# Optimization experiments

Hardware: AMD Instinct MI355X
Metric: run time of the kernel (lower is better)

The kernel has to match this reference:

```python
import jax, jax.numpy as jnp
import numpy as np

E = 1024      # embed_dim
H = 16        # num_heads
HD = E // H   # head_dim = 64


def setup_inputs() -> dict:
    key = jax.random.key(0)
    ks = jax.random.split(key, 8)
    T, B, S = 1024, 4, 1024
    return {
        "query": jax.random.normal(ks[0], (T, B, E), jnp.float32),
        "key": jax.random.normal(ks[1], (S, B, E), jnp.float32),
        "value": jax.random.normal(ks[2], (S, B, E), jnp.float32),
        "attn_mask": jax.random.normal(ks[3], (T, S), jnp.float32),
        "key_padding_mask": jax.random.randint(ks[4], (B, S), 0, 2, jnp.int32),
        "in_proj_weight": jax.random.normal(ks[5], (3 * E, E), jnp.float32) * 0.02,
        "in_proj_bias": jnp.zeros((3 * E,), jnp.float32),
        "out_w": jax.random.normal(ks[6], (E, E), jnp.float32) * 0.02,
        "out_b": jnp.zeros((E,), jnp.float32),
    }


def reference(query, key, value, attn_mask, key_padding_mask,
              in_proj_weight, in_proj_bias, out_w, out_b):
    T, B, _ = query.shape
    S = key.shape[0]
    w_q, w_k, w_v = jnp.split(in_proj_weight, 3, axis=0)   # each [E, E]
    b_q, b_k, b_v = jnp.split(in_proj_bias, 3, axis=0)
    q = query @ w_q.T + b_q                                # [T, B, E]
    k = key @ w_k.T + b_k                                  # [S, B, E]
    v = value @ w_v.T + b_v                                # [S, B, E]
    # [len, B, E] -> [B*H, len, HD]
    q = q.reshape(T, B * H, HD).transpose(1, 0, 2) / jnp.sqrt(jnp.float32(HD))
    k = k.reshape(S, B * H, HD).transpose(1, 0, 2)
    v = v.reshape(S, B * H, HD).transpose(1, 0, 2)
    scores = jnp.einsum('bth,bsh->bts', q, k)              # [B*H, T, S]
    scores = scores + attn_mask[None]                      # float additive mask
    pad = key_padding_mask.astype(bool)                    # [B, S]
    pad = jnp.broadcast_to(pad[:, None, None, :], (B, H, 1, S)).reshape(B * H, 1, S)
    scores = jnp.where(pad, -jnp.inf, scores)
    weights = jax.nn.softmax(scores, axis=-1)              # dropout p=0 -> identity
    out = jnp.einsum('bts,bsh->bth', weights, v)           # [B*H, T, HD]
    out = out.transpose(1, 0, 2).reshape(T, B, E)
    out = out @ out_w.T + out_b
    weights_avg = weights.reshape(B, H, T, S).mean(axis=1) # sum/H == mean
    return out, weights_avg
```

## Files before the change

kernel.cpp:

```cpp
#include <hip/hip_runtime.h>
#include <stdint.h>

typedef short bf16x8 __attribute__((ext_vector_type(8)));
typedef float f32x4  __attribute__((ext_vector_type(4)));

#define LOG2E_F 1.4426950408889634f
#define QSCALE_F 0.1803368801111204f

__device__ __forceinline__ unsigned short f2bf(float f) {
    unsigned int u = __float_as_uint(f);
    return (unsigned short)((u + 0x7FFFu + ((u >> 16) & 1u)) >> 16);
}

__device__ __forceinline__ unsigned short f2bfu(float f) {
    return (unsigned short)((__float_as_uint(f) + 0x8000u) >> 16);
}

__device__ __forceinline__ uint4 pack8(float4 a, float4 b) {
    union { unsigned short us[8]; uint4 v; } p;
    p.us[0] = f2bf(a.x); p.us[1] = f2bf(a.y); p.us[2] = f2bf(a.z); p.us[3] = f2bf(a.w);
    p.us[4] = f2bf(b.x); p.us[5] = f2bf(b.y); p.us[6] = f2bf(b.z); p.us[7] = f2bf(b.w);
    return p.v;
}

__global__ __launch_bounds__(256)
void cvt_kernel(const float* __restrict__ q, const float* __restrict__ k,
                const float* __restrict__ v, const float* __restrict__ w,
                const float* __restrict__ ow,
                uint4* __restrict__ Xb, uint4* __restrict__ Wb, uint4* __restrict__ OWb)
{
    const unsigned g = blockIdx.x * 256 + threadIdx.x;
    const float* src;
    uint4* dst;
    if (g < 1572864u) {
        dst = Xb + g;
        if (g < 524288u)        src = q + (size_t)g * 8;
        else if (g < 1048576u)  src = k + (size_t)(g - 524288u) * 8;
        else                    src = v + (size_t)(g - 1048576u) * 8;
    } else if (g < 1966080u) {
        src = w + (size_t)(g - 1572864u) * 8;
        dst = Wb + (g - 1572864u);
    } else {
        src = ow + (size_t)(g - 1966080u) * 8;
        dst = OWb + (g - 1966080u);
    }
    float4 a = *(const float4*)src;
    float4 b = *(const float4*)(src + 4);
    *dst = pack8(a, b);
}

__global__ __launch_bounds__(256)
void mtr_kernel(const float* __restrict__ m, float* __restrict__ mt)
{
    __shared__ float tile[64][65];
    const int bt = (blockIdx.x & 15) << 6;
    const int bs = (blockIdx.x >> 4) << 6;
    const int tx = threadIdx.x & 63;
    const int ty = threadIdx.x >> 6;
#pragma unroll
    for (int i = 0; i < 64; i += 4)
        tile[ty + i][tx] = m[(size_t)(bt + ty + i) * 1024 + bs + tx];
    __syncthreads();
#pragma unroll
    for (int i = 0; i < 64; i += 4)
        mt[(size_t)(bs + ty + i) * 1024 + bt + tx] = tile[tx][ty + i];
}

__global__ __launch_bounds__(256)
void qkv_proj_kernel(const unsigned short* __restrict__ Xb, const unsigned short* __restrict__ Wb,
                     const float* __restrict__ bias,
                     unsigned short* __restrict__ Qb, unsigned short* __restrict__ Kb,
                     unsigned short* __restrict__ Vtb)
{
    const int z = blockIdx.z;
    const int j   = blockIdx.x;
    const int xcd = j & 7, idx = j >> 3;
    const int row0 = ((xcd << 2) + (idx >> 3)) * 128;
    const int col0 = (idx & 7) * 128;
    const int wofs = z << 10;

    const unsigned short* A = Xb + (size_t)z * 4194304;
    const unsigned short* B = Wb;

    __shared__ __align__(16) unsigned short As[128 * 72];
    __shared__ __align__(16) unsigned short Bs[128 * 72];

    const int tid  = threadIdx.x;
    const int lane = tid & 63;
    const int wv   = tid >> 6;
    const int wr   = wv >> 1, wc = wv & 1;

    const f32x4 zero4 = {0.f, 0.f, 0.f, 0.f};
    f32x4 acc[4][4];
#pragma unroll
    for (int m = 0; m < 4; ++m)
#pragma unroll
        for (int n = 0; n < 4; ++n) acc[m][n] = zero4;

    const int srow = tid >> 1;
    const int scol = (tid & 1) << 5;
    const int arow = wr * 64 + (lane & 15);
    const int brow = wc * 64 + (lane & 15);
    const int kof  = (lane >> 4) << 3;

    const unsigned short* pa = A + (size_t)(row0 + srow) * 1024 + scol;
    const unsigned short* pb = B + (size_t)(wofs + col0 + srow) * 1024 + scol;
    uint4 ra0 = *(const uint4*)(pa + 0),  ra1 = *(const uint4*)(pa + 8);
    uint4 ra2 = *(const uint4*)(pa + 16), ra3 = *(const uint4*)(pa + 24);
    uint4 rb0 = *(const uint4*)(pb + 0),  rb1 = *(const uint4*)(pb + 8);
    uint4 rb2 = *(const uint4*)(pb + 16), rb3 = *(const uint4*)(pb + 24);

    for (int k0 = 0; k0 < 1024; k0 += 64) {
        __syncthreads();
        *(uint4*)&As[srow * 72 + scol]      = ra0;
        *(uint4*)&As[srow * 72 + scol + 8]  = ra1;
        *(uint4*)&As[srow * 72 + scol + 16] = ra2;
        *(uint4*)&As[srow * 72 + scol + 24] = ra3;
        *(uint4*)&Bs[srow * 72 + scol]      = rb0;
        *(uint4*)&Bs[srow * 72 + scol + 8]  = rb1;
        *(uint4*)&Bs[srow * 72 + scol + 16] = rb2;
        *(uint4*)&Bs[srow * 72 + scol + 24] = rb3;
        __syncthreads();

        if (k0 < 960) {
            pa = A + (size_t)(row0 + srow) * 1024 + k0 + 64 + scol;
            pb = B + (size_t)(wofs + col0 + srow) * 1024 + k0 + 64 + scol;
            ra0 = *(const uint4*)(pa + 0);  ra1 = *(const uint4*)(pa + 8);
            ra2 = *(const uint4*)(pa + 16); ra3 = *(const uint4*)(pa + 24);
            rb0 = *(const uint4*)(pb + 0);  rb1 = *(const uint4*)(pb + 8);
            rb2 = *(const uint4*)(pb + 16); rb3 = *(const uint4*)(pb + 24);
        }

#pragma unroll
        for (int kk = 0; kk < 2; ++kk) {
            bf16x8 af[4], bfr[4];
#pragma unroll
            for (int m = 0; m < 4; ++m)
                af[m] = *(const bf16x8*)&As[(arow + m * 16) * 72 + kk * 32 + kof];
#pragma unroll
            for (int n = 0; n < 4; ++n)
                bfr[n] = *(const bf16x8*)&Bs[(brow + n * 16) * 72 + kk * 32 + kof];
#pragma unroll
            for (int m = 0; m < 4; ++m)
#pragma unroll
                for (int n = 0; n < 4; ++n)
                    acc[m][n] = __builtin_amdgcn_mfma_f32_16x16x32_bf16(af[m], bfr[n], acc[m][n], 0, 0, 0);
        }
    }

    const int ccol = lane & 15;
    const int crow = (lane >> 4) << 2;
#pragma unroll
    for (int n = 0; n < 4; ++n) {
        const int gc   = col0 + wc * 64 + n * 16 + ccol;
        const float bv = bias[wofs + gc];
        const int head = gc >> 6, d = gc & 63;
#pragma unroll
        for (int m = 0; m < 4; ++m) {
#pragma unroll
            for (int r = 0; r < 4; ++r) {
                const int gr = row0 + wr * 64 + m * 16 + crow + r;
                const int t  = gr >> 2, b = gr & 3;
                const int bh = (b << 4) + head;
                float vv = acc[m][n][r] + bv;
                if (z == 0)      Qb [((size_t)bh << 16) + ((size_t)t << 6) + d]  = f2bf(vv * QSCALE_F);
                else if (z == 1) Kb [((size_t)bh << 16) + ((size_t)t << 6) + d]  = f2bf(vv);
                else             Vtb[((size_t)bh << 16) + ((size_t)d << 10) + t] = f2bf(vv);
            }
        }
    }
}

__global__ __launch_bounds__(512)
void flash_kernel(const unsigned short* __restrict__ Qb, const unsigned short* __restrict__ Kb,
                  const unsigned short* __restrict__ Vtb, const float* __restrict__ maskT,
                  const int* __restrict__ padmask,
                  float* __restrict__ rl_buf, unsigned short* __restrict__ attn_out)
{
    const int j   = blockIdx.x;
    const int xcd = j & 7, idx = j >> 3;
    const int bh  = xcd * 8 + (idx >> 3);
    const int t0  = (idx & 7) << 7;
    const int b   = bh >> 4, h = bh & 15;

    __shared__ __align__(16) unsigned short Ks[2][2][64 * 72];
    __shared__ __align__(16) unsigned short Vs[2][2][64 * 72];

    const int tid  = threadIdx.x;
    const int lane = tid & 63;
    const int wv   = tid >> 6;
    const int kof  = (lane >> 4) << 3;
    const int c16  = lane & 15;
    const int g4   = (lane >> 4) << 2;

    const unsigned short* Qbase = Qb  + ((size_t)bh << 16);
    const unsigned short* Kbase = Kb  + ((size_t)bh << 16);
    const unsigned short* Vbase = Vtb + ((size_t)bh << 16);

    bf16x8 qf[2];
#pragma unroll
    for (int kk = 0; kk < 2; ++kk)
        qf[kk] = *(const bf16x8*)(Qbase + ((size_t)(t0 + wv * 16 + c16) << 6) + kk * 32 + kof);

    const bf16x8 ones = {16256, 16256, 16256, 16256, 16256, 16256, 16256, 16256};

    const f32x4 zero4 = {0.f, 0.f, 0.f, 0.f};
    f32x4 acco[4];
#pragma unroll
    for (int nd = 0; nd < 4; ++nd) acco[nd] = zero4;
    f32x4 acc_l = zero4;

    const int srow_st = tid >> 3;
    const int scol_st = (tid & 7) << 3;

    const int bb  = scol_st & 31;
    const int hh  = scol_st & 32;
    const int cL  = hh + ((bb & 15) >> 2) * 8 + (bb >> 4) * 4;
    const int bb4 = bb + 4;
    const int cH  = hh + ((bb4 & 15) >> 2) * 8 + (bb4 >> 4) * 4;

    const int tr2 = t0 + wv * 16 + c16;

    const unsigned short* kp = Kbase + ((size_t)srow_st << 6) + scol_st;
    const unsigned short* vp = Vbase + ((size_t)srow_st << 10) + scol_st;
    uint4 kA = *(const uint4*)kp;
    uint4 kB = *(const uint4*)(kp + 4096);
    uint4 vA = *(const uint4*)vp;
    uint4 vB = *(const uint4*)(vp + 64);

    {
        *(uint4*)&Ks[0][0][srow_st * 72 + scol_st] = kA;
        *(uint4*)&Ks[0][1][srow_st * 72 + scol_st] = kB;
        uint2 lo, hi;
        lo.x = vA.x; lo.y = vA.y; hi.x = vA.z; hi.y = vA.w;
        *(uint2*)&Vs[0][0][srow_st * 72 + cL] = lo;
        *(uint2*)&Vs[0][0][srow_st * 72 + cH] = hi;
        lo.x = vB.x; lo.y = vB.y; hi.x = vB.z; hi.y = vB.w;
        *(uint2*)&Vs[0][1][srow_st * 72 + cL] = lo;
        *(uint2*)&Vs[0][1][srow_st * 72 + cH] = hi;
    }
    kp = Kbase + ((size_t)(128 + srow_st) << 6) + scol_st;
    vp = Vbase + ((size_t)srow_st << 10) + 128 + scol_st;
    kA = *(const uint4*)kp;
    kB = *(const uint4*)(kp + 4096);
    vA = *(const uint4*)vp;
    vB = *(const uint4*)(vp + 64);
    __syncthreads();

    for (int rd = 0; rd < 8; ++rd) {
        const int cur = rd & 1;
        const int s0  = rd << 7;

        if (rd < 7) {
            *(uint4*)&Ks[cur ^ 1][0][srow_st * 72 + scol_st] = kA;
            *(uint4*)&Ks[cur ^ 1][1][srow_st * 72 + scol_st] = kB;
            uint2 lo, hi;
            lo.x = vA.x; lo.y = vA.y; hi.x = vA.z; hi.y = vA.w;
            *(uint2*)&Vs[cur ^ 1][0][srow_st * 72 + cL] = lo;
            *(uint2*)&Vs[cur ^ 1][0][srow_st * 72 + cH] = hi;
            lo.x = vB.x; lo.y = vB.y; hi.x = vB.z; hi.y = vB.w;
            *(uint2*)&Vs[cur ^ 1][1][srow_st * 72 + cL] = lo;
            *(uint2*)&Vs[cur ^ 1][1][srow_st * 72 + cH] = hi;
        }
        if (rd < 6) {
            const int sn = s0 + 256;
            kp = Kbase + ((size_t)(sn + srow_st) << 6) + scol_st;
            vp = Vbase + ((size_t)srow_st << 10) + sn + scol_st;
            kA = *(const uint4*)kp;
            kB = *(const uint4*)(kp + 4096);
            vA = *(const uint4*)vp;
            vB = *(const uint4*)(vp + 64);
        }

        f32x4 accsA[4], accsB[4];
#pragma unroll
        for (int n = 0; n < 4; ++n) { accsA[n] = zero4; accsB[n] = zero4; }
        __builtin_amdgcn_s_setprio(1);
#pragma unroll
        for (int n = 0; n < 4; ++n) {
            bf16x8 kfA0 = *(const bf16x8*)&Ks[cur][0][(n * 16 + c16) * 72 + kof];
            bf16x8 kfA1 = *(const bf16x8*)&Ks[cur][0][(n * 16 + c16) * 72 + 32 + kof];
            accsA[n] = __builtin_amdgcn_mfma_f32_16x16x32_bf16(kfA0, qf[0], accsA[n], 0, 0, 0);
            accsA[n] = __builtin_amdgcn_mfma_f32_16x16x32_bf16(kfA1, qf[1], accsA[n], 0, 0, 0);
            bf16x8 kfB0 = *(const bf16x8*)&Ks[cur][1][(n * 16 + c16) * 72 + kof];
            bf16x8 kfB1 = *(const bf16x8*)&Ks[cur][1][(n * 16 + c16) * 72 + 32 + kof];
            accsB[n] = __builtin_amdgcn_mfma_f32_16x16x32_bf16(kfB0, qf[0], accsB[n], 0, 0, 0);
            accsB[n] = __builtin_amdgcn_mfma_f32_16x16x32_bf16(kfB1, qf[1], accsB[n], 0, 0, 0);
        }
        __builtin_amdgcn_s_setprio(0);

#pragma unroll
        for (int tile = 0; tile < 2; ++tile) {
            const int s0t = s0 + tile * 64;
            f32x4* accs = tile ? accsB : accsA;

            float mk[4][4];
            int4 pd[4];
#pragma unroll
            for (int n = 0; n < 4; ++n) {
                const int srow = s0t + n * 16 + g4;
                pd[n] = *(const int4*)(padmask + (b << 10) + srow);
#pragma unroll
                for (int r = 0; r < 4; ++r)
                    mk[n][r] = maskT[(size_t)(srow + r) * 1024 + tr2];
            }

            union { unsigned short us[16]; bf16x8 v[2]; } pk;
#pragma unroll
            for (int n = 0; n < 4; ++n) {
                float x0 = fmaf(mk[n][0], LOG2E_F, accs[n][0]);
                float x1 = fmaf(mk[n][1], LOG2E_F, accs[n][1]);
                float x2 = fmaf(mk[n][2], LOG2E_F, accs[n][2]);
                float x3 = fmaf(mk[n][3], LOG2E_F, accs[n][3]);
                if (pd[n].x) x0 = -1e30f;
                if (pd[n].y) x1 = -1e30f;
                if (pd[n].z) x2 = -1e30f;
                if (pd[n].w) x3 = -1e30f;
                pk.us[n * 4 + 0] = f2bfu(__builtin_amdgcn_exp2f(x0));
                pk.us[n * 4 + 1] = f2bfu(__builtin_amdgcn_exp2f(x1));
                pk.us[n * 4 + 2] = f2bfu(__builtin_amdgcn_exp2f(x2));
                pk.us[n * 4 + 3] = f2bfu(__builtin_amdgcn_exp2f(x3));
            }

            __builtin_amdgcn_s_setprio(1);
#pragma unroll
            for (int hhh = 0; hhh < 2; ++hhh) {
                bf16x8 pf = pk.v[hhh];
#pragma unroll
                for (int nd = 0; nd < 4; ++nd) {
                    bf16x8 vf = *(const bf16x8*)&Vs[cur][tile][(nd * 16 + c16) * 72 + hhh * 32 + kof];
                    acco[nd] = __builtin_amdgcn_mfma_f32_16x16x32_bf16(pf, vf, acco[nd], 0, 0, 0);
                }
                acc_l = __builtin_amdgcn_mfma_f32_16x16x32_bf16(pf, ones, acc_l, 0, 0, 0);
            }
            __builtin_amdgcn_s_setprio(0);
        }

        if (rd < 7) __syncthreads();
    }

#pragma unroll
    for (int r = 0; r < 4; ++r) {
        const int t = t0 + wv * 16 + g4 + r;
        const float rl = 1.0f / acc_l[r];
        if (c16 == 0)
            rl_buf[(bh << 10) + t] = rl;
#pragma unroll
        for (int nd = 0; nd < 4; ++nd) {
            const int d = nd * 16 + c16;
            attn_out[((size_t)t * 4 + b) * 1024 + h * 64 + d] = f2bf(acco[nd][r] * rl);
        }
    }
}

__global__ __launch_bounds__(256)
void wavg_kernel(const unsigned short* __restrict__ Qb, const unsigned short* __restrict__ Kb,
                 const float* __restrict__ attn_mask, const int* __restrict__ padmask,
                 const float* __restrict__ rl_buf, float* __restrict__ wout)
{
    const int j   = blockIdx.x;
    const int xcd = j & 7;
    const int b   = xcd >> 1;
    const int rr  = ((j >> 3) << 1) + (xcd & 1);
    const int t0  = (rr >> 4) << 6;
    const int s0  = (rr & 15) << 6;

    __shared__ __align__(16) unsigned short Qs[64 * 72];
    __shared__ __align__(16) unsigned short Ks2[64 * 72];

    const int tid  = threadIdx.x;
    const int lane = tid & 63;
    const int wv   = tid >> 6;
    const int wr   = wv >> 1, wc = wv & 1;
    const int kof  = (lane >> 4) << 3;
    const int srow_st = tid >> 2;
    const int scol_st = (tid & 3) << 4;

    const int t_base = t0 + wr * 32 + ((lane >> 4) << 2);
    const int s_base = s0 + wc * 32 + (lane & 15);

    int pad2[2];
#pragma unroll
    for (int nn = 0; nn < 2; ++nn) pad2[nn] = padmask[(b << 10) + s_base + nn * 16];

    float maskv[2][2][4];
#pragma unroll
    for (int mm = 0; mm < 2; ++mm)
#pragma unroll
        for (int r = 0; r < 4; ++r)
#pragma unroll
            for (int nn = 0; nn < 2; ++nn)
                maskv[mm][nn][r] = attn_mask[(size_t)(t_base + mm * 16 + r) * 1024 + s_base + nn * 16] * LOG2E_F;

    float wsum[2][2][4];
#pragma unroll
    for (int mm = 0; mm < 2; ++mm)
#pragma unroll
        for (int nn = 0; nn < 2; ++nn)
#pragma unroll
            for (int r = 0; r < 4; ++r) wsum[mm][nn][r] = 0.f;

    for (int h = 0; h < 16; ++h) {
        const int bh = (b << 4) + h;
        __syncthreads();
        {
            const unsigned short* qp = Qb + ((size_t)bh << 16) + ((size_t)(t0 + srow_st) << 6) + scol_st;
            *(uint4*)&Qs[srow_st * 72 + scol_st]     = *(const uint4*)qp;
            *(uint4*)&Qs[srow_st * 72 + scol_st + 8] = *(const uint4*)(qp + 8);
            const unsigned short* kp = Kb + ((size_t)bh << 16) + ((size_t)(s0 + srow_st) << 6) + scol_st;
            *(uint4*)&Ks2[srow_st * 72 + scol_st]     = *(const uint4*)kp;
            *(uint4*)&Ks2[srow_st * 72 + scol_st + 8] = *(const uint4*)(kp + 8);
        }
        __syncthreads();

        float rlv[2][4];
#pragma unroll
        for (int mm = 0; mm < 2; ++mm)
#pragma unroll
            for (int r = 0; r < 4; ++r)
                rlv[mm][r] = rl_buf[(bh << 10) + t_base + mm * 16 + r];

        const f32x4 zero4 = {0.f, 0.f, 0.f, 0.f};
        f32x4 accs[2][2];
#pragma unroll
        for (int mm = 0; mm < 2; ++mm)
#pragma unroll
            for (int nn = 0; nn < 2; ++nn) accs[mm][nn] = zero4;
#pragma unroll
        for (int nn = 0; nn < 2; ++nn) {
            bf16x8 kf0 = *(const bf16x8*)&Ks2[(wc * 32 + nn * 16 + (lane & 15)) * 72 + kof];
            bf16x8 kf1 = *(const bf16x8*)&Ks2[(wc * 32 + nn * 16 + (lane & 15)) * 72 + 32 + kof];
#pragma unroll
            for (int mm = 0; mm < 2; ++mm) {
                bf16x8 qf0 = *(const bf16x8*)&Qs[(wr * 32 + mm * 16 + (lane & 15)) * 72 + kof];
                bf16x8 qf1 = *(const bf16x8*)&Qs[(wr * 32 + mm * 16 + (lane & 15)) * 72 + 32 + kof];
                accs[mm][nn] = __builtin_amdgcn_mfma_f32_16x16x32_bf16(qf0, kf0, accs[mm][nn], 0, 0, 0);
                accs[mm][nn] = __builtin_amdgcn_mfma_f32_16x16x32_bf16(qf1, kf1, accs[mm][nn], 0, 0, 0);
            }
        }
#pragma unroll
        for (int mm = 0; mm < 2; ++mm)
#pragma unroll
            for (int nn = 0; nn < 2; ++nn)
#pragma unroll
                for (int r = 0; r < 4; ++r)
                    if (!pad2[nn]) {
                        float x = accs[mm][nn][r] + maskv[mm][nn][r];
                        wsum[mm][nn][r] += __builtin_amdgcn_exp2f(x) * rlv[mm][r];
                    }
    }

#pragma unroll
    for (int mm = 0; mm < 2; ++mm)
#pragma unroll
        for (int nn = 0; nn < 2; ++nn)
#pragma unroll
            for (int r = 0; r < 4; ++r)
                wout[((size_t)b << 20) + (size_t)(t_base + mm * 16 + r) * 1024 + s_base + nn * 16]
                    = wsum[mm][nn][r] * 0.0625f;
}

__global__ __launch_bounds__(256)
void out_proj_kernel(const unsigned short* __restrict__ A, const unsigned short* __restrict__ Wb,
                     const float* __restrict__ bias, float* __restrict__ out)
{
    const int j   = blockIdx.x;
    const int xcd = j & 7, idx = j >> 3;
    const int row0 = ((xcd << 2) + (idx >> 3)) * 128;
    const int col0 = (idx & 7) * 128;

    __shared__ __align__(16) unsigned short As[128 * 72];
    __shared__ __align__(16) unsigned short Bs[128 * 72];

    const int tid  = threadIdx.x;
    const int lane = tid & 63;
    const int wv   = tid >> 6;
    const int wr   = wv >> 1, wc = wv & 1;

    const f32x4 zero4 = {0.f, 0.f, 0.f, 0.f};
    f32x4 acc[4][4];
#pragma unroll
    for (int m = 0; m < 4; ++m)
#pragma unroll
        for (int n = 0; n < 4; ++n) acc[m][n] = zero4;

    const int srow = tid >> 1;
    const int scol = (tid & 1) << 5;
    const int arow = wr * 64 + (lane & 15);
    const int brow = wc * 64 + (lane & 15);
    const int kof  = (lane >> 4) << 3;

    const unsigned short* pa = A  + (size_t)(row0 + srow) * 1024 + scol;
    const unsigned short* pb = Wb + (size_t)(col0 + srow) * 1024 + scol;
    uint4 ra0 = *(const uint4*)(pa + 0),  ra1 = *(const uint4*)(pa + 8);
    uint4 ra2 = *(const uint4*)(pa + 16), ra3 = *(const uint4*)(pa + 24);
    uint4 rb0 = *(const uint4*)(pb + 0),  rb1 = *(const uint4*)(pb + 8);
    uint4 rb2 = *(const uint4*)(pb + 16), rb3 = *(const uint4*)(pb + 24);

    for (int k0 = 0; k0 < 1024; k0 += 64) {
        __syncthreads();
        *(uint4*)&As[srow * 72 + scol]      = ra0;
        *(uint4*)&As[srow * 72 + scol + 8]  = ra1;
        *(uint4*)&As[srow * 72 + scol + 16] = ra2;
        *(uint4*)&As[srow * 72 + scol + 24] = ra3;
        *(uint4*)&Bs[srow * 72 + scol]      = rb0;
        *(uint4*)&Bs[srow * 72 + scol + 8]  = rb1;
        *(uint4*)&Bs[srow * 72 + scol + 16] = rb2;
        *(uint4*)&Bs[srow * 72 + scol + 24] = rb3;
        __syncthreads();

        if (k0 < 960) {
            pa = A  + (size_t)(row0 + srow) * 1024 + k0 + 64 + scol;
            pb = Wb + (size_t)(col0 + srow) * 1024 + k0 + 64 + scol;
            ra0 = *(const uint4*)(pa + 0);  ra1 = *(const uint4*)(pa + 8);
            ra2 = *(const uint4*)(pa + 16); ra3 = *(const uint4*)(pa + 24);
            rb0 = *(const uint4*)(pb + 0);  rb1 = *(const uint4*)(pb + 8);
            rb2 = *(const uint4*)(pb + 16); rb3 = *(const uint4*)(pb + 24);
        }

#pragma unroll
        for (int kk = 0; kk < 2; ++kk) {
            bf16x8 af[4], bfr[4];
#pragma unroll
            for (int m = 0; m < 4; ++m)
                af[m] = *(const bf16x8*)&As[(arow + m * 16) * 72 + kk * 32 + kof];
#pragma unroll
            for (int n = 0; n < 4; ++n)
                bfr[n] = *(const bf16x8*)&Bs[(brow + n * 16) * 72 + kk * 32 + kof];
#pragma unroll
            for (int m = 0; m < 4; ++m)
#pragma unroll
                for (int n = 0; n < 4; ++n)
                    acc[m][n] = __builtin_amdgcn_mfma_f32_16x16x32_bf16(af[m], bfr[n], acc[m][n], 0, 0, 0);
        }
    }

    const int ccol = lane & 15;
    const int crow = (lane >> 4) << 2;
#pragma unroll
    for (int n = 0; n < 4; ++n) {
        const int gc   = col0 + wc * 64 + n * 16 + ccol;
        const float bv = bias[gc];
#pragma unroll
        for (int m = 0; m < 4; ++m) {
#pragma unroll
            for (int r = 0; r < 4; ++r) {
                const int gr = row0 + wr * 64 + m * 16 + crow + r;
                out[(size_t)gr * 1024 + gc] = acc[m][n][r] + bv;
            }
        }
    }
}

extern "C" void kernel_launch(void* const* d_in, const int* in_sizes, int n_in,
                              void* d_out, int out_size, void* d_ws, size_t ws_size,
                              hipStream_t stream)
{
    const float* query     = (const float*)d_in[0];
    const float* key       = (const float*)d_in[1];
    const float* value     = (const float*)d_in[2];
    const float* attn_mask = (const float*)d_in[3];
    const int*   padmask   = (const int*)  d_in[4];
    const float* in_proj_w = (const float*)d_in[5];
    const float* in_proj_b = (const float*)d_in[6];
    const float* out_w     = (const float*)d_in[7];
    const float* out_b     = (const float*)d_in[8];

    float* out  = (float*)d_out;
    float* wavg = out + 4194304;

    char* ws = (char*)d_ws;
    unsigned short* Qb     = (unsigned short*)(ws);
    unsigned short* Kb     = (unsigned short*)(ws + 8388608);
    unsigned short* Vtb    = (unsigned short*)(ws + 16777216);
    unsigned short* Xb     = (unsigned short*)(ws + 25165824);
    unsigned short* attn_o = (unsigned short*)(ws + 25165824);
    float*          maskT  = (float*)(ws + 33554432);
    unsigned short* Wb     = (unsigned short*)(ws + 50331648);
    unsigned short* OWb    = (unsigned short*)(ws + 56623104);
    float*          rl_buf = (float*)(ws + 58720256);

    cvt_kernel<<<dim3(8192), 256, 0, stream>>>(query, key, value, in_proj_w, out_w,
                                               (uint4*)Xb, (uint4*)Wb, (uint4*)OWb);
    qkv_proj_kernel<<<dim3(256, 1, 3), 256, 0, stream>>>(Xb, Wb, in_proj_b, Qb, Kb, Vtb);
    mtr_kernel<<<dim3(256), 256, 0, stream>>>(attn_mask, maskT);
    flash_kernel<<<dim3(512), 512, 0, stream>>>(Qb, Kb, Vtb, maskT, padmask,
                                                rl_buf, attn_o);
    wavg_kernel<<<dim3(1024), 256, 0, stream>>>(Qb, Kb, attn_mask, padmask,
                                                rl_buf, wavg);
    out_proj_kernel<<<dim3(256), 256, 0, stream>>>(attn_o, OWb, out_b, out);
}
```

Before: 156.2 us.

## Interleave transposed mask layout for vector loads and double-buffer wavg Q/K tiles

The mask transpose kernel now writes an interleaved layout that groups four consecutive s rows per t, so the attention kernel fetches its four mask values with one float4 load instead of four strided scalar loads. The wavg kernel double-buffers the Q/K shared tiles, keeping the next head's data in registers and cutting the barriers per head from two to one, so global loads overlap with MFMA and exp work. The cost is twice the shared memory in wavg and extra live registers, which may lower occupancy.

```diff
diff --git a/kernel.cpp b/kernel.cpp
--- a/kernel.cpp
+++ b/kernel.cpp
@@ -62,8 +62,10 @@
         tile[ty + i][tx] = m[(size_t)(bt + ty + i) * 1024 + bs + tx];
     __syncthreads();
 #pragma unroll
-    for (int i = 0; i < 64; i += 4)
-        mt[(size_t)(bs + ty + i) * 1024 + bt + tx] = tile[tx][ty + i];
+    for (int i = 0; i < 64; i += 4) {
+        const int s = bs + ty + i;
+        mt[(size_t)(s >> 2) * 4096 + (bt + tx) * 4 + (s & 3)] = tile[tx][ty + i];
+    }
 }
 
 __global__ __launch_bounds__(256)
@@ -294,24 +296,22 @@
             const int s0t = s0 + tile * 64;
             f32x4* accs = tile ? accsB : accsA;
 
-            float mk[4][4];
+            float4 mk[4];
             int4 pd[4];
 #pragma unroll
             for (int n = 0; n < 4; ++n) {
                 const int srow = s0t + n * 16 + g4;
                 pd[n] = *(const int4*)(padmask + (b << 10) + srow);
-#pragma unroll
-                for (int r = 0; r < 4; ++r)
-                    mk[n][r] = maskT[(size_t)(srow + r) * 1024 + tr2];
+                mk[n] = *(const float4*)(maskT + (size_t)(srow >> 2) * 4096 + tr2 * 4);
             }
 
             union { unsigned short us[16]; bf16x8 v[2]; } pk;
 #pragma unroll
             for (int n = 0; n < 4; ++n) {
-                float x0 = fmaf(mk[n][0], LOG2E_F, accs[n][0]);
-                float x1 = fmaf(mk[n][1], LOG2E_F, accs[n][1]);
-                float x2 = fmaf(mk[n][2], LOG2E_F, accs[n][2]);
-                float x3 = fmaf(mk[n][3], LOG2E_F, accs[n][3]);
+                float x0 = fmaf(mk[n].x, LOG2E_F, accs[n][0]);
+                float x1 = fmaf(mk[n].y, LOG2E_F, accs[n][1]);
+                float x2 = fmaf(mk[n].z, LOG2E_F, accs[n][2]);
+                float x3 = fmaf(mk[n].w, LOG2E_F, accs[n][3]);
                 if (pd[n].x) x0 = -1e30f;
                 if (pd[n].y) x1 = -1e30f;
                 if (pd[n].z) x2 = -1e30f;
@@ -365,8 +365,8 @@
     const int t0  = (rr >> 4) << 6;
     const int s0  = (rr & 15) << 6;
 
-    __shared__ __align__(16) unsigned short Qs[64 * 72];
-    __shared__ __align__(16) unsigned short Ks2[64 * 72];
+    __shared__ __align__(16) unsigned short Qs[2][64 * 72];
+    __shared__ __align__(16) unsigned short Ks2[2][64 * 72];
 
     const int tid  = threadIdx.x;
     const int lane = tid & 63;
@@ -400,18 +400,42 @@
 #pragma unroll
             for (int r = 0; r < 4; ++r) wsum[mm][nn][r] = 0.f;
 
+    const unsigned short* qsrc = Qb + ((size_t)(t0 + srow_st) << 6) + scol_st;
+    const unsigned short* ksrc = Kb + ((size_t)(s0 + srow_st) << 6) + scol_st;
+    const size_t bh0 = (size_t)(b << 4) << 16;
+
+    uint4 q0 = *(const uint4*)(qsrc + bh0);
+    uint4 q1 = *(const uint4*)(qsrc + bh0 + 8);
+    uint4 k0 = *(const uint4*)(ksrc + bh0);
+    uint4 k1 = *(const uint4*)(ksrc + bh0 + 8);
+    *(uint4*)&Qs[0][srow_st * 72 + scol_st]      = q0;
+    *(uint4*)&Qs[0][srow_st * 72 + scol_st + 8]  = q1;
+    *(uint4*)&Ks2[0][srow_st * 72 + scol_st]     = k0;
+    *(uint4*)&Ks2[0][srow_st * 72 + scol_st + 8] = k1;
+    q0 = *(const uint4*)(qsrc + bh0 + 65536);
+    q1 = *(const uint4*)(qsrc + bh0 + 65536 + 8);
+    k0 = *(const uint4*)(ksrc + bh0 + 65536);
+    k1 = *(const uint4*)(ksrc + bh0 + 65536 + 8);
+    __syncthreads();
+
+#pragma unroll 2
     for (int h = 0; h < 16; ++h) {
-        const int bh = (b << 4) + h;
-        __syncthreads();
-        {
-            const unsigned short* qp = Qb + ((size_t)bh << 16) + ((size_t)(t0 + srow_st) << 6) + scol_st;
-            *(uint4*)&Qs[srow_st * 72 + scol_st]     = *(const uint4*)qp;
-            *(uint4*)&Qs[srow_st * 72 + scol_st + 8] = *(const uint4*)(qp + 8);
-            const unsigned short* kp = Kb + ((size_t)bh << 16) + ((size_t)(s0 + srow_st) << 6) + scol_st;
-            *(uint4*)&Ks2[srow_st * 72 + scol_st]     = *(const uint4*)kp;
-            *(uint4*)&Ks2[srow_st * 72 + scol_st + 8] = *(const uint4*)(kp + 8);
-        }
-        __syncthreads();
+        const int cur = h & 1;
+        const int bh  = (b << 4) + h;
+
+        if (h < 15) {
+            *(uint4*)&Qs[cur ^ 1][srow_st * 72 + scol_st]      = q0;
+            *(uint4*)&Qs[cur ^ 1][srow_st * 72 + scol_st + 8]  = q1;
+            *(uint4*)&Ks2[cur ^ 1][srow_st * 72 + scol_st]     = k0;
+            *(uint4*)&Ks2[cur ^ 1][srow_st * 72 + scol_st + 8] = k1;
+        }
+        if (h < 14) {
+            const size_t of = bh0 + (size_t)(h + 2) * 65536;
+            q0 = *(const uint4*)(qsrc + of);
+            q1 = *(const uint4*)(qsrc + of + 8);
+            k0 = *(const uint4*)(ksrc + of);
+            k1 = *(const uint4*)(ksrc + of + 8);
+        }
 
         float rlv[2][4];
 #pragma unroll
@@ -428,12 +452,12 @@
             for (int nn = 0; nn < 2; ++nn) accs[mm][nn] = zero4;
 #pragma unroll
         for (int nn = 0; nn < 2; ++nn) {
-            bf16x8 kf0 = *(const bf16x8*)&Ks2[(wc * 32 + nn * 16 + (lane & 15)) * 72 + kof];
-            bf16x8 kf1 = *(const bf16x8*)&Ks2[(wc * 32 + nn * 16 + (lane & 15)) * 72 + 32 + kof];
+            bf16x8 kf0 = *(const bf16x8*)&Ks2[cur][(wc * 32 + nn * 16 + (lane & 15)) * 72 + kof];
+            bf16x8 kf1 = *(const bf16x8*)&Ks2[cur][(wc * 32 + nn * 16 + (lane & 15)) * 72 + 32 + kof];
 #pragma unroll
             for (int mm = 0; mm < 2; ++mm) {
-                bf16x8 qf0 = *(const bf16x8*)&Qs[(wr * 32 + mm * 16 + (lane & 15)) * 72 + kof];
-                bf16x8 qf1 = *(const bf16x8*)&Qs[(wr * 32 + mm * 16 + (lane & 15)) * 72 + 32 + kof];
+                bf16x8 qf0 = *(const bf16x8*)&Qs[cur][(wr * 32 + mm * 16 + (lane & 15)) * 72 + kof];
+                bf16x8 qf1 = *(const bf16x8*)&Qs[cur][(wr * 32 + mm * 16 + (lane & 15)) * 72 + 32 + kof];
                 accs[mm][nn] = __builtin_amdgcn_mfma_f32_16x16x32_bf16(qf0, kf0, accs[mm][nn], 0, 0, 0);
                 accs[mm][nn] = __builtin_amdgcn_mfma_f32_16x16x32_bf16(qf1, kf1, accs[mm][nn], 0, 0, 0);
             }
@@ -448,6 +472,8 @@
                         float x = accs[mm][nn][r] + maskv[mm][nn][r];
                         wsum[mm][nn][r] += __builtin_amdgcn_exp2f(x) * rlv[mm][r];
                     }
+
+        if (h < 15) __syncthreads();
     }
 
 #pragma unroll
```

Result: no change. 154.7 us (-1.0%).
